# Kernel optimization log

Measured on AMD Instinct MI355X. Metric: run time of the kernel, lower is better.

The kernel has to match this reference:

```python
import jax, jax.numpy as jnp
import numpy as np

B, S, D_IN = 2, 2048, 1024
H, DA, DH = 16, 64, 64          # num_heads, attention_dim, head_dim (linear_hidden_dim)
EMBED = 1024
KSIZE = 1


def causal_conv1d(x_bsc, w):
    """x_bsc: (B,S,Cin); w: (Cout,Cin,K). Left-pad K-1 -> causal. Returns (B,Cout,S)."""
    k = w.shape[-1]
    x_bcs = jnp.transpose(x_bsc, (0, 2, 1))
    x_bcs = jnp.pad(x_bcs, ((0, 0), (0, 0), (k - 1, 0)))
    return jax.lax.conv_general_dilated(
        x_bcs, w, window_strides=(1,), padding='VALID',
        dimension_numbers=('NCH', 'OIH', 'NCH'))


def setup_inputs() -> dict:
    key = jax.random.key(0)
    ks = jax.random.split(key, 7)
    x = jax.random.normal(ks[0], (B, S, D_IN), dtype=jnp.float32)
    # causal mask: 1 where attended, 0 where masked (masked_fill where ==0)
    attn_mask = jnp.tril(jnp.ones((S, S), dtype=jnp.int32))[None, None]  # (1,1,S,S)
    wq = 0.02 * jax.random.normal(ks[1], (H * DA, D_IN, KSIZE), dtype=jnp.float32)
    wk = 0.02 * jax.random.normal(ks[2], (H * DA, D_IN, KSIZE), dtype=jnp.float32)
    wv = 0.02 * jax.random.normal(ks[3], (H * DH, D_IN, KSIZE), dtype=jnp.float32)
    w_out = 0.02 * jax.random.normal(ks[4], (EMBED, H * DH), dtype=jnp.float32)
    b_out = 0.02 * jax.random.normal(ks[5], (EMBED,), dtype=jnp.float32)
    return {"x": x, "attn_mask": attn_mask, "wq": wq, "wk": wk, "wv": wv,
            "w_out": w_out, "b_out": b_out}


def reference(x, attn_mask, wq, wk, wv, w_out, b_out):
    b, s, _ = x.shape
    scale = DH ** (-0.5)  # NOTE: torch code scales by head_dim, not attention_dim
    q = causal_conv1d(x, wq)  # (B, H*DA, S)
    k = causal_conv1d(x, wk)  # (B, H*DA, S)
    v = causal_conv1d(x, wv)  # (B, H*DH, S)
    q = q.reshape(b, H, DA, s).transpose(0, 1, 3, 2)  # (B,H,S,DA)
    k = k.reshape(b, H, DA, s).transpose(0, 1, 3, 2)
    v = v.reshape(b, H, DH, s).transpose(0, 1, 3, 2)  # (B,H,S,DH)
    scores = scale * jnp.einsum('bhnd,bhmd->bhnm', q, k)
    scores = jnp.where(attn_mask == 0, -jnp.inf, scores)
    probs = jax.nn.softmax(scores, axis=-1)
    context = jnp.einsum('bhnm,bhmd->bhnd', probs, v)  # (B,H,S,DH)
    context = context.transpose(0, 2, 1, 3).reshape(b, s, H * DH)
    return context @ w_out.T + b_out
```

## Files before the change

### kernel.cpp

```cpp
#include <hip/hip_runtime.h>
#include <math.h>


typedef __bf16 bf16;
typedef __bf16 bf16x8 __attribute__((ext_vector_type(8)));
typedef __bf16 bf16x4 __attribute__((ext_vector_type(4)));
typedef float  f32x4  __attribute__((ext_vector_type(4)));

#define MFMA16(a, b, c) __builtin_amdgcn_mfma_f32_16x16x32_bf16((a), (b), (c), 0, 0, 0)

__device__ __forceinline__ void gll16(const void* g, void* l) {
    __builtin_amdgcn_global_load_lds(
        (__attribute__((address_space(1))) unsigned int*)g,
        (__attribute__((address_space(3))) unsigned int*)l, 16, 0, 0);
}

__global__ __launch_bounds__(256) void cvt_all_kernel(
    const float* __restrict__ x,  const float* __restrict__ wq,
    const float* __restrict__ wk, const float* __restrict__ wv,
    const float* __restrict__ wo,
    bf16* __restrict__ xb,  bf16* __restrict__ wqb, bf16* __restrict__ wkb,
    bf16* __restrict__ wvb, bf16* __restrict__ wob)
{
    const int blk = blockIdx.x;
    const float* src; bf16* dst; int off; float scale = 1.f;
    if (blk < 4096)      { src = x;  dst = xb;  off = blk * 1024; }
    else if (blk < 5120) { src = wq; dst = wqb; off = (blk - 4096) * 1024;
                           scale = 0.18033688011112042f; }
    else if (blk < 6144) { src = wk; dst = wkb; off = (blk - 5120) * 1024; }
    else if (blk < 7168) { src = wv; dst = wvb; off = (blk - 6144) * 1024; }
    else                 { src = wo; dst = wob; off = (blk - 7168) * 1024; }
    const int i = off + threadIdx.x * 4;
    f32x4 v = *(const f32x4*)(src + i);
    bf16x4 o;
    o[0] = (bf16)(v[0] * scale); o[1] = (bf16)(v[1] * scale);
    o[2] = (bf16)(v[2] * scale); o[3] = (bf16)(v[3] * scale);
    *(bf16x4*)(dst + i) = o;
}

__global__ __launch_bounds__(256, 3) void qkv_mfma_kernel(
    const bf16* __restrict__ xb, const bf16* __restrict__ wqb,
    const bf16* __restrict__ wkb, const bf16* __restrict__ wvb,
    bf16* __restrict__ Qb, bf16* __restrict__ Kb, bf16* __restrict__ Vtb)
{
    __shared__ bf16 As[2][128 * 32];
    __shared__ bf16 Bs[2][128 * 32];
    const int mt = blockIdx.x;
    const int nt = blockIdx.y;
    const int which = nt >> 3;
    const bf16* Wm = (which == 0) ? wqb : (which == 1) ? wkb : wvb;

    const int t = threadIdx.x;
    const int w = t >> 6, lane = t & 63, quad = lane >> 4, l16 = lane & 15;
    const int wm = (w >> 1) * 64, wn = (w & 1) * 64;
    const int srow = lane >> 2;
    const int scol = (lane & 3) * 8;

    const bf16* Ab = xb + ((size_t)(mt * 128) + srow) * 1024 + scol;
    const bf16* Bb = Wm + ((size_t)((nt & 7) * 128) + srow) * 1024 + scol;

    f32x4 acc[4][4];
    #pragma unroll
    for (int i = 0; i < 4; i++)
        #pragma unroll
        for (int j = 0; j < 4; j++)
            #pragma unroll
            for (int r = 0; r < 4; r++) acc[i][j][r] = 0.f;

    gll16(Ab + (size_t)(w * 16) * 1024,       As[0] + w * 512);
    gll16(Ab + (size_t)((w + 4) * 16) * 1024, As[0] + (w + 4) * 512);
    gll16(Bb + (size_t)(w * 16) * 1024,       Bs[0] + w * 512);
    gll16(Bb + (size_t)((w + 4) * 16) * 1024, Bs[0] + (w + 4) * 512);

    for (int it = 0; it < 32; it++) {
        const int cur = it & 1, nxt = cur ^ 1;
        __syncthreads();
        if (it < 31) {
            const int kn = it * 32 + 32;
            gll16(Ab + (size_t)(w * 16) * 1024 + kn,       As[nxt] + w * 512);
            gll16(Ab + (size_t)((w + 4) * 16) * 1024 + kn, As[nxt] + (w + 4) * 512);
            gll16(Bb + (size_t)(w * 16) * 1024 + kn,       Bs[nxt] + w * 512);
            gll16(Bb + (size_t)((w + 4) * 16) * 1024 + kn, Bs[nxt] + (w + 4) * 512);
        }
        bf16x8 af[4], bfr[4];
        #pragma unroll
        for (int i = 0; i < 4; i++)
            af[i] = *(const bf16x8*)&As[cur][(wm + i * 16 + l16) * 32 + quad * 8];
        #pragma unroll
        for (int j = 0; j < 4; j++)
            bfr[j] = *(const bf16x8*)&Bs[cur][(wn + j * 16 + l16) * 32 + quad * 8];
        #pragma unroll
        for (int i = 0; i < 4; i++)
            #pragma unroll
            for (int j = 0; j < 4; j++)
                acc[i][j] = MFMA16(af[i], bfr[j], acc[i][j]);
    }

    const int nbase = (nt & 7) * 128 + wn;
    if (which == 2) {
        #pragma unroll
        for (int i = 0; i < 4; i++) {
            const int m0 = mt * 128 + wm + i * 16 + quad * 4;
            const int bb = m0 >> 11, s0 = m0 & 2047;
            #pragma unroll
            for (int j = 0; j < 4; j++) {
                const int n = nbase + j * 16 + l16;
                const int h = n >> 6, d = n & 63;
                bf16x4 pk;
                #pragma unroll
                for (int r = 0; r < 4; r++) pk[r] = (bf16)acc[i][j][r];
                *(bf16x4*)&Vtb[(((size_t)(bb * 16 + h)) * 64 + d) * 2048 + s0] = pk;
            }
        }
    } else {
        bf16* Out = (which == 0) ? Qb : Kb;
        #pragma unroll
        for (int i = 0; i < 4; i++) {
            #pragma unroll
            for (int r = 0; r < 4; r++) {
                const int m = mt * 128 + wm + i * 16 + quad * 4 + r;
                const int bb = m >> 11, s = m & 2047;
                #pragma unroll
                for (int j = 0; j < 4; j++) {
                    const int n = nbase + j * 16 + l16;
                    const int h = n >> 6, d = n & 63;
                    Out[(((size_t)(bb * 16 + h)) * 2048 + s) * 64 + d] =
                        (bf16)acc[i][j][r];
                }
            }
        }
    }
}

__global__ __launch_bounds__(256, 2) void attn_mfma_kernel(
    const bf16* __restrict__ Qb, const bf16* __restrict__ Kb,
    const bf16* __restrict__ Vtb, bf16* __restrict__ ctxb)
{
    __shared__ bf16 Ks[2][128 * 64];
    __shared__ bf16 Vts[2][64 * 128];
    __shared__ bf16 Pl[4][16 * 128];

    const int id = blockIdx.x;
    const int bh = id & 31;
    const int pr = id >> 5;
    const int qa = pr, qb = 31 - pr;
    const int h = bh & 15, b = bh >> 4;
    const int t = threadIdx.x;
    const int w = t >> 6, lane = t & 63, quad = lane >> 4, l16 = lane & 15;

    const size_t hb = (size_t)(b * 16 + h);
    const bf16* Qh = Qb + hb * (2048 * 64);
    const bf16* Kh = Kb + hb * (2048 * 64);
    const bf16* Vh = Vtb + hb * (64 * 2048);

    bf16x8 qf0[2], qf1[2];
    {
        const bf16* Qr0 = Qh + (size_t)(qa * 64 + w * 16 + l16) * 64;
        qf0[0] = *(const bf16x8*)(Qr0 + quad * 8);
        qf0[1] = *(const bf16x8*)(Qr0 + 32 + quad * 8);
        const bf16* Qr1 = Qh + (size_t)(qb * 64 + w * 16 + l16) * 64;
        qf1[0] = *(const bf16x8*)(Qr1 + quad * 8);
        qf1[1] = *(const bf16x8*)(Qr1 + 32 + quad * 8);
    }

    bf16x8 ones;
    #pragma unroll
    for (int i = 0; i < 8; i++) ones[i] = (bf16)1.0f;

    f32x4 o0[4], o1[4], l0, l1;
    #pragma unroll
    for (int r = 0; r < 4; r++) { l0[r] = 0.f; l1[r] = 0.f; }
    #pragma unroll
    for (int dt = 0; dt < 4; dt++)
        #pragma unroll
        for (int r = 0; r < 4; r++) { o0[dt][r] = 0.f; o1[dt][r] = 0.f; }

    const int ksr = lane >> 3, ksc = lane & 7;
    const int vsr = lane >> 4, vsc = lane & 15;

    #define STAGE(ktv, buf)                                                   \
        {                                                                     \
            _Pragma("unroll")                                                 \
            for (int j = 0; j < 4; j++) {                                     \
                const int c = 4 * w + j;                                      \
                const int kr = c * 8 + ksr;                                   \
                gll16(Kh + (size_t)((ktv) * 128 + kr) * 64 +                  \
                          ((ksc ^ (kr & 7)) * 8),                             \
                      Ks[buf] + c * 512);                                     \
                const int vr = c * 4 + vsr;                                   \
                gll16(Vh + (size_t)vr * 2048 + (ktv) * 128 +                  \
                          ((vsc ^ (vr & 15)) * 8),                            \
                      Vts[buf] + c * 512);                                    \
            }                                                                 \
        }

    #define ITER(qt64, ktv, diag, qfv, oacc, lacc, cur)                       \
        {                                                                     \
            f32x4 sacc[8];                                                    \
            _Pragma("unroll")                                                 \
            for (int tt = 0; tt < 8; tt++) {                                  \
                _Pragma("unroll")                                             \
                for (int r = 0; r < 4; r++) sacc[tt][r] = 0.f;                \
                const int krow = tt * 16 + l16;                               \
                bf16x8 kf0 = *(const bf16x8*)&Ks[cur][krow * 64 +             \
                                 ((quad)     ^ (krow & 7)) * 8];              \
                bf16x8 kf1 = *(const bf16x8*)&Ks[cur][krow * 64 +             \
                                 ((quad + 4) ^ (krow & 7)) * 8];              \
                sacc[tt] = MFMA16(kf0, (qfv)[0], sacc[tt]);                   \
                sacc[tt] = MFMA16(kf1, (qfv)[1], sacc[tt]);                   \
            }                                                                 \
            const int qrow = (qt64) * 64 + w * 16 + l16;                      \
            _Pragma("unroll")                                                 \
            for (int tt = 0; tt < 8; tt++) {                                  \
                bf16x4 pk;                                                    \
                _Pragma("unroll")                                             \
                for (int r = 0; r < 4; r++) {                                 \
                    float p = __builtin_amdgcn_exp2f(sacc[tt][r]);            \
                    if ((diag) && ((ktv) * 128 + tt * 16 + quad * 4 + r) > qrow) \
                        p = 0.f;                                              \
                    pk[r] = (bf16)p;                                          \
                }                                                             \
                const int cs = (tt * 2 + (quad >> 1)) ^ l16;                  \
                *(bf16x4*)&Pl[w][l16 * 128 + cs * 8 + (quad & 1) * 4] = pk;   \
            }                                                                 \
            bf16x8 ap[4];                                                     \
            _Pragma("unroll")                                                 \
            for (int u = 0; u < 4; u++) {                                     \
                ap[u] = *(const bf16x8*)&Pl[w][l16 * 128 +                    \
                             ((quad + 4 * u) ^ l16) * 8];                     \
                (lacc) = MFMA16(ap[u], ones, (lacc));                         \
            }                                                                 \
            _Pragma("unroll")                                                 \
            for (int dt = 0; dt < 4; dt++) {                                  \
                const int drow = dt * 16 + l16;                               \
                _Pragma("unroll")                                             \
                for (int u = 0; u < 4; u++) {                                 \
                    bf16x8 bv = *(const bf16x8*)&Vts[cur][drow * 128 +        \
                                     ((4 * u + quad) ^ (drow & 15)) * 8];     \
                    (oacc)[dt] = MFMA16(ap[u], bv, (oacc)[dt]);               \
                }                                                             \
            }                                                                 \
        }

    const int na = (qa >> 1) + 1;
    STAGE(0, 0);

    for (int v = 0; v < 17; v++) {
        const int cur = v & 1, nxt = cur ^ 1;
        __syncthreads();
        if (v < 16) {
            const int vn = v + 1;
            const int ktn = (vn < na) ? vn : vn - na;
            STAGE(ktn, nxt);
        }
        if (v < na) {
            ITER(qa, v, (v == na - 1), qf0, o0, l0, cur);
        } else {
            const int kt = v - na;
            ITER(qb, kt, (v == 16), qf1, o1, l1, cur);
        }
    }
    #undef STAGE
    #undef ITER

    #pragma unroll
    for (int r = 0; r < 4; r++) {
        const float inv0 = 1.f / l0[r];
        const int s0 = qa * 64 + w * 16 + quad * 4 + r;
        const float inv1 = 1.f / l1[r];
        const int s1 = qb * 64 + w * 16 + quad * 4 + r;
        #pragma unroll
        for (int dt = 0; dt < 4; dt++) {
            ctxb[((size_t)(b * 2048 + s0)) * 1024 + h * 64 + dt * 16 + l16] =
                (bf16)(o0[dt][r] * inv0);
            ctxb[((size_t)(b * 2048 + s1)) * 1024 + h * 64 + dt * 16 + l16] =
                (bf16)(o1[dt][r] * inv1);
        }
    }
}

__global__ __launch_bounds__(256, 2) void oproj_mfma_kernel(
    const bf16* __restrict__ ctxb, const bf16* __restrict__ wob,
    const float* __restrict__ b_out, float* __restrict__ out)
{
    __shared__ bf16 As[2][64 * 32];
    __shared__ bf16 Bs[2][128 * 32];
    const int mt = blockIdx.x;
    const int nt = blockIdx.y;
    const int t = threadIdx.x;
    const int w = t >> 6, lane = t & 63, quad = lane >> 4, l16 = lane & 15;
    const int srow = lane >> 2;
    const int scol = (lane & 3) * 8;

    const bf16* Ab = ctxb + (size_t)(mt * 64 + srow) * 1024 + scol;
    const bf16* Bb = wob + (size_t)(nt * 128 + srow) * 1024 + scol;

    f32x4 acc[8];
    #pragma unroll
    for (int j = 0; j < 8; j++)
        #pragma unroll
        for (int r = 0; r < 4; r++) acc[j][r] = 0.f;

    gll16(Ab + (size_t)(w * 16) * 1024,       As[0] + w * 512);
    gll16(Bb + (size_t)(w * 16) * 1024,       Bs[0] + w * 512);
    gll16(Bb + (size_t)((w + 4) * 16) * 1024, Bs[0] + (w + 4) * 512);

    for (int it = 0; it < 32; it++) {
        const int cur = it & 1, nxt = cur ^ 1;
        __syncthreads();
        if (it < 31) {
            const int kn = it * 32 + 32;
            gll16(Ab + (size_t)(w * 16) * 1024 + kn,       As[nxt] + w * 512);
            gll16(Bb + (size_t)(w * 16) * 1024 + kn,       Bs[nxt] + w * 512);
            gll16(Bb + (size_t)((w + 4) * 16) * 1024 + kn, Bs[nxt] + (w + 4) * 512);
        }
        bf16x8 af = *(const bf16x8*)&As[cur][(w * 16 + l16) * 32 + quad * 8];
        #pragma unroll
        for (int j = 0; j < 8; j++) {
            bf16x8 bfr = *(const bf16x8*)&Bs[cur][(j * 16 + l16) * 32 + quad * 8];
            acc[j] = MFMA16(af, bfr, acc[j]);
        }
    }

    #pragma unroll
    for (int j = 0; j < 8; j++)
        #pragma unroll
        for (int r = 0; r < 4; r++) {
            const int m = mt * 64 + w * 16 + quad * 4 + r;
            const int n = nt * 128 + j * 16 + l16;
            out[(size_t)m * 1024 + n] = acc[j][r] + b_out[n];
        }
}

extern "C" void kernel_launch(void* const* d_in, const int* in_sizes, int n_in,
                              void* d_out, int out_size, void* d_ws, size_t ws_size,
                              hipStream_t stream)
{
    const float* x     = (const float*)d_in[0];
    const float* wq    = (const float*)d_in[2];
    const float* wk    = (const float*)d_in[3];
    const float* wv    = (const float*)d_in[4];
    const float* w_out = (const float*)d_in[5];
    const float* b_out = (const float*)d_in[6];
    float* out = (float*)d_out;

    char* ws = (char*)d_ws;
    bf16* xb   = (bf16*)(ws);
    bf16* wqb  = (bf16*)(ws + (8u  << 20));
    bf16* wkb  = (bf16*)(ws + (10u << 20));
    bf16* wvb  = (bf16*)(ws + (12u << 20));
    bf16* wob  = (bf16*)(ws + (14u << 20));
    bf16* Qb   = (bf16*)(ws + (16u << 20));
    bf16* Kb   = (bf16*)(ws + (24u << 20));
    bf16* Vtb  = (bf16*)(ws + (32u << 20));
    bf16* ctxb = (bf16*)(ws + (40u << 20));

    cvt_all_kernel<<<8192, 256, 0, stream>>>(x, wq, wk, wv, w_out,
                                             xb, wqb, wkb, wvb, wob);
    qkv_mfma_kernel<<<dim3(32, 24), 256, 0, stream>>>(xb, wqb, wkb, wvb, Qb, Kb, Vtb);
    attn_mfma_kernel<<<512, 256, 0, stream>>>(Qb, Kb, Vtb, ctxb);
    oproj_mfma_kernel<<<dim3(64, 8), 256, 0, stream>>>(ctxb, wob, b_out, out);
}
```

Before: 188.8 us.

## Batch convert blocks, XCD-swizzle QKV grid, setprio in attention, 2x4 oproj warp tiles

The conversion kernel now has each block handle four 1024-element chunks, with a quarter as many blocks. The QKV GEMM remaps block indices so blocks landing on the same XCD share weight column tiles, aiming for better L2 reuse. The attention loop raises wave priority around its MFMA sections with s_setprio. The output projection switches each warp from a 16x128 strip to a 32x64 tile, so fewer LDS B-fragment reads are needed per MFMA. These are several independent tweaks, each with modest and uncertain effect.

```diff
diff --git a/kernel.cpp b/kernel.cpp
--- a/kernel.cpp
+++ b/kernel.cpp
@@ -22,20 +22,23 @@
     bf16* __restrict__ xb,  bf16* __restrict__ wqb, bf16* __restrict__ wkb,
     bf16* __restrict__ wvb, bf16* __restrict__ wob)
 {
-    const int blk = blockIdx.x;
-    const float* src; bf16* dst; int off; float scale = 1.f;
-    if (blk < 4096)      { src = x;  dst = xb;  off = blk * 1024; }
-    else if (blk < 5120) { src = wq; dst = wqb; off = (blk - 4096) * 1024;
-                           scale = 0.18033688011112042f; }
-    else if (blk < 6144) { src = wk; dst = wkb; off = (blk - 5120) * 1024; }
-    else if (blk < 7168) { src = wv; dst = wvb; off = (blk - 6144) * 1024; }
-    else                 { src = wo; dst = wob; off = (blk - 7168) * 1024; }
-    const int i = off + threadIdx.x * 4;
-    f32x4 v = *(const f32x4*)(src + i);
-    bf16x4 o;
-    o[0] = (bf16)(v[0] * scale); o[1] = (bf16)(v[1] * scale);
-    o[2] = (bf16)(v[2] * scale); o[3] = (bf16)(v[3] * scale);
-    *(bf16x4*)(dst + i) = o;
+    #pragma unroll
+    for (int k = 0; k < 4; k++) {
+        const int blk = blockIdx.x * 4 + k;
+        const float* src; bf16* dst; int off; float scale = 1.f;
+        if (blk < 4096)      { src = x;  dst = xb;  off = blk * 1024; }
+        else if (blk < 5120) { src = wq; dst = wqb; off = (blk - 4096) * 1024;
+                               scale = 0.18033688011112042f; }
+        else if (blk < 6144) { src = wk; dst = wkb; off = (blk - 5120) * 1024; }
+        else if (blk < 7168) { src = wv; dst = wvb; off = (blk - 6144) * 1024; }
+        else                 { src = wo; dst = wob; off = (blk - 7168) * 1024; }
+        const int i = off + threadIdx.x * 4;
+        f32x4 v = *(const f32x4*)(src + i);
+        bf16x4 o;
+        o[0] = (bf16)(v[0] * scale); o[1] = (bf16)(v[1] * scale);
+        o[2] = (bf16)(v[2] * scale); o[3] = (bf16)(v[3] * scale);
+        *(bf16x4*)(dst + i) = o;
+    }
 }
 
 __global__ __launch_bounds__(256, 3) void qkv_mfma_kernel(
@@ -45,8 +48,11 @@
 {
     __shared__ bf16 As[2][128 * 32];
     __shared__ bf16 Bs[2][128 * 32];
-    const int mt = blockIdx.x;
-    const int nt = blockIdx.y;
+    const int lin = blockIdx.x + 32 * blockIdx.y;
+    const int xcd = lin & 7, lid = lin >> 3;
+    const int rem = xcd * 96 + lid;
+    const int mt = rem & 31;
+    const int nt = rem >> 5;
     const int which = nt >> 3;
     const bf16* Wm = (which == 0) ? wqb : (which == 1) ? wkb : wvb;
 
@@ -197,6 +203,7 @@
     #define ITER(qt64, ktv, diag, qfv, oacc, lacc, cur)                       \
         {                                                                     \
             f32x4 sacc[8];                                                    \
+            __builtin_amdgcn_s_setprio(1);                                    \
             _Pragma("unroll")                                                 \
             for (int tt = 0; tt < 8; tt++) {                                  \
                 _Pragma("unroll")                                             \
@@ -209,6 +216,7 @@
                 sacc[tt] = MFMA16(kf0, (qfv)[0], sacc[tt]);                   \
                 sacc[tt] = MFMA16(kf1, (qfv)[1], sacc[tt]);                   \
             }                                                                 \
+            __builtin_amdgcn_s_setprio(0);                                    \
             const int qrow = (qt64) * 64 + w * 16 + l16;                      \
             _Pragma("unroll")                                                 \
             for (int tt = 0; tt < 8; tt++) {                                  \
@@ -224,6 +232,7 @@
                 *(bf16x4*)&Pl[w][l16 * 128 + cs * 8 + (quad & 1) * 4] = pk;   \
             }                                                                 \
             bf16x8 ap[4];                                                     \
+            __builtin_amdgcn_s_setprio(1);                                    \
             _Pragma("unroll")                                                 \
             for (int u = 0; u < 4; u++) {                                     \
                 ap[u] = *(const bf16x8*)&Pl[w][l16 * 128 +                    \
@@ -240,6 +249,7 @@
                     (oacc)[dt] = MFMA16(ap[u], bv, (oacc)[dt]);               \
                 }                                                             \
             }                                                                 \
+            __builtin_amdgcn_s_setprio(0);                                    \
         }
 
     const int na = (qa >> 1) + 1;
@@ -295,11 +305,16 @@
     const bf16* Ab = ctxb + (size_t)(mt * 64 + srow) * 1024 + scol;
     const bf16* Bb = wob + (size_t)(nt * 128 + srow) * 1024 + scol;
 
-    f32x4 acc[8];
-    #pragma unroll
-    for (int j = 0; j < 8; j++)
-        #pragma unroll
-        for (int r = 0; r < 4; r++) acc[j][r] = 0.f;
+    const int wrow = (w >> 1) * 32;
+    const int wcol = (w & 1) * 64;
+
+    f32x4 acc[2][4];
+    #pragma unroll
+    for (int i = 0; i < 2; i++)
+        #pragma unroll
+        for (int j = 0; j < 4; j++)
+            #pragma unroll
+            for (int r = 0; r < 4; r++) acc[i][j][r] = 0.f;
 
     gll16(Ab + (size_t)(w * 16) * 1024,       As[0] + w * 512);
     gll16(Bb + (size_t)(w * 16) * 1024,       Bs[0] + w * 512);
@@ -314,22 +329,26 @@
             gll16(Bb + (size_t)(w * 16) * 1024 + kn,       Bs[nxt] + w * 512);
             gll16(Bb + (size_t)((w + 4) * 16) * 1024 + kn, Bs[nxt] + (w + 4) * 512);
         }
-        bf16x8 af = *(const bf16x8*)&As[cur][(w * 16 + l16) * 32 + quad * 8];
-        #pragma unroll
-        for (int j = 0; j < 8; j++) {
-            bf16x8 bfr = *(const bf16x8*)&Bs[cur][(j * 16 + l16) * 32 + quad * 8];
-            acc[j] = MFMA16(af, bfr, acc[j]);
-        }
-    }
-
-    #pragma unroll
-    for (int j = 0; j < 8; j++)
-        #pragma unroll
-        for (int r = 0; r < 4; r++) {
-            const int m = mt * 64 + w * 16 + quad * 4 + r;
-            const int n = nt * 128 + j * 16 + l16;
-            out[(size_t)m * 1024 + n] = acc[j][r] + b_out[n];
-        }
+        bf16x8 af0 = *(const bf16x8*)&As[cur][(wrow + l16) * 32 + quad * 8];
+        bf16x8 af1 = *(const bf16x8*)&As[cur][(wrow + 16 + l16) * 32 + quad * 8];
+        #pragma unroll
+        for (int j = 0; j < 4; j++) {
+            bf16x8 bv = *(const bf16x8*)&Bs[cur][(wcol + j * 16 + l16) * 32 + quad * 8];
+            acc[0][j] = MFMA16(af0, bv, acc[0][j]);
+            acc[1][j] = MFMA16(af1, bv, acc[1][j]);
+        }
+    }
+
+    #pragma unroll
+    for (int i = 0; i < 2; i++)
+        #pragma unroll
+        for (int j = 0; j < 4; j++)
+            #pragma unroll
+            for (int r = 0; r < 4; r++) {
+                const int m = mt * 64 + wrow + i * 16 + quad * 4 + r;
+                const int n = nt * 128 + wcol + j * 16 + l16;
+                out[(size_t)m * 1024 + n] = acc[i][j][r] + b_out[n];
+            }
 }
 
 extern "C" void kernel_launch(void* const* d_in, const int* in_sizes, int n_in,
@@ -355,7 +374,7 @@
     bf16* Vtb  = (bf16*)(ws + (32u << 20));
     bf16* ctxb = (bf16*)(ws + (40u << 20));
 
-    cvt_all_kernel<<<8192, 256, 0, stream>>>(x, wq, wk, wv, w_out,
+    cvt_all_kernel<<<2048, 256, 0, stream>>>(x, wq, wk, wv, w_out,
                                              xb, wqb, wkb, wvb, wob);
     qkv_mfma_kernel<<<dim3(32, 24), 256, 0, stream>>>(xb, wqb, wkb, wvb, Qb, Kb, Vtb);
     attn_mfma_kernel<<<512, 256, 0, stream>>>(Qb, Kb, Vtb, ctxb);
```

Result: no change. 187.1 us (-0.9%).
